# Kernel tuning notes

Measured on AMD Instinct MI355X. Metric: run time of the kernel, lower is better.

## Reference

```python
import jax, jax.numpy as jnp
import numpy as np
from jax import lax

N_PROT = 20000
N_DRUG = 4000
IN_DRUG = 4000
IN_PROT = 64
N_ET = 128
N_BASE = 32
N_EMBED = 48
PD_DIM = 16
H1 = 32
H2 = 16
RGCN_IN = N_EMBED + PD_DIM  # mod='cat'
E_PP = 800000
E_DP = 400000
E_DD = 1000000


def seg_mean(vals, idx, n):
    s = jax.ops.segment_sum(vals, idx, num_segments=n)
    c = jax.ops.segment_sum(jnp.ones(idx.shape, vals.dtype), idx, num_segments=n)
    return s / jnp.maximum(c, 1.0)[:, None]


def gcn(x, W, b, edge_index, n):
    # GCNConv with self-loops and symmetric normalization
    src, dst = edge_index[0], edge_index[1]
    h = x @ W
    deg = jax.ops.segment_sum(jnp.ones(src.shape, h.dtype), dst, num_segments=n) + 1.0
    dis = lax.rsqrt(deg)
    msg = h[src] * (dis[src] * dis[dst])[:, None]
    agg = jax.ops.segment_sum(msg, dst, num_segments=n) + h * (dis * dis)[:, None]
    return agg + b


def rgcn(x, edge_index, etype, att, basis, root, n):
    # message_e = x[src_e] @ (att[etype_e] @ basis) = sum_b att[etype_e, b] * (x[src_e] @ basis[b])
    src, dst = edge_index[0], edge_index[1]
    x_j = x[src]  # [E, in]
    a = att[etype]  # [E, B]
    init = jnp.zeros((src.shape[0], basis.shape[-1]), x.dtype)

    def body(carry, ba):
        basis_b, a_b = ba  # [in,out], [E]
        return carry + a_b[:, None] * (x_j @ basis_b), None

    msgs, _ = lax.scan(body, init, (basis, a.T))
    return seg_mean(msgs, dst, n) + x @ root


def setup_inputs() -> dict:
    key = jax.random.key(0)
    ks = jax.random.split(key, 24)
    x_drug = jax.random.uniform(ks[0], (N_DRUG, IN_DRUG), dtype=jnp.float32)
    d_norm = jax.random.uniform(ks[1], (N_DRUG,), dtype=jnp.float32) + 0.5
    x_prot = jax.random.normal(ks[2], (N_PROT, IN_PROT), dtype=jnp.float32)
    pp_edge_index = jax.random.randint(ks[3], (2, E_PP), 0, N_PROT, dtype=jnp.int32)
    dp_src = jax.random.randint(ks[4], (E_DP,), 0, N_PROT, dtype=jnp.int32)
    dp_dst = N_PROT + jax.random.randint(ks[5], (E_DP,), 0, N_DRUG, dtype=jnp.int32)
    dp_edge_index = jnp.stack([dp_src, dp_dst])
    dp_range_list = jnp.zeros((N_DRUG, 2), dtype=jnp.int32)  # unused in math
    dd_edge_index = jax.random.randint(ks[6], (2, E_DD), 0, N_DRUG, dtype=jnp.int32)
    dd_edge_type = jnp.sort(jax.random.randint(ks[7], (E_DD,), 0, N_ET, dtype=jnp.int32))
    et_np = np.asarray(dd_edge_type)
    starts = np.searchsorted(et_np, np.arange(N_ET), side='left')
    ends = np.searchsorted(et_np, np.arange(N_ET), side='right')
    dd_range_list = jnp.asarray(np.stack([starts, ends], axis=1), dtype=jnp.int32)
    # parameters (init scales per reset_parameters)
    embed = jax.random.normal(ks[8], (IN_DRUG, N_EMBED), dtype=jnp.float32)
    W1 = jax.random.normal(ks[9], (IN_PROT, H1), dtype=jnp.float32) / np.sqrt(IN_PROT)
    b1 = jnp.zeros((H1,), jnp.float32)
    W2 = jax.random.normal(ks[10], (H1, H2), dtype=jnp.float32) / np.sqrt(H1)
    b2 = jnp.zeros((H2,), jnp.float32)
    hg_weight = jax.random.normal(ks[11], (H2, PD_DIM), dtype=jnp.float32) / np.sqrt(H2)
    att1 = jax.random.normal(ks[12], (N_ET, N_BASE), dtype=jnp.float32) / np.sqrt(N_BASE)
    basis1 = jax.random.normal(ks[13], (N_BASE, RGCN_IN, H1), dtype=jnp.float32) / np.sqrt(RGCN_IN)
    root1 = jax.random.normal(ks[14], (RGCN_IN, H1), dtype=jnp.float32) / np.sqrt(RGCN_IN)
    att2 = jax.random.normal(ks[15], (N_ET, N_BASE), dtype=jnp.float32) / np.sqrt(N_BASE)
    basis2 = jax.random.normal(ks[16], (N_BASE, H1, H2), dtype=jnp.float32) * (2.0 / H1)
    root2 = jax.random.normal(ks[17], (H1, H2), dtype=jnp.float32) * (2.0 / H1)
    return {
        'x_drug': x_drug, 'd_norm': d_norm, 'x_prot': x_prot,
        'pp_edge_index': pp_edge_index, 'dp_edge_index': dp_edge_index,
        'dp_range_list': dp_range_list, 'dd_edge_index': dd_edge_index,
        'dd_edge_type': dd_edge_type, 'dd_range_list': dd_range_list,
        'embed': embed, 'W1': W1, 'b1': b1, 'W2': W2, 'b2': b2,
        'hg_weight': hg_weight, 'att1': att1, 'basis1': basis1, 'root1': root1,
        'att2': att2, 'basis2': basis2, 'root2': root2,
    }


def reference(x_drug, d_norm, x_prot, pp_edge_index, dp_edge_index, dp_range_list,
              dd_edge_index, dd_edge_type, dd_range_list, embed, W1, b1, W2, b2,
              hg_weight, att1, basis1, root1, att2, basis2, root2):
    # PPEncoder: two GCN layers
    xp = jax.nn.relu(gcn(x_prot, W1, b1, pp_edge_index, N_PROT))
    xp = gcn(xp, W2, b2, pp_edge_index, N_PROT)  # [N_PROT, H2]
    # MyHierarchyConv: concat zero drug rows, mean-aggregate prot->drug, project
    xcat = jnp.concatenate([xp, jnp.zeros((N_DRUG, H2), xp.dtype)], axis=0)
    agg = seg_mean(xcat[dp_edge_index[0]], dp_edge_index[1], N_PROT + N_DRUG)
    xp_drug = agg[N_PROT:] @ hg_weight  # [N_DRUG, PD_DIM]
    # drug embedding + normalization, concat ('cat' mode)
    xd = (x_drug @ embed) / d_norm[:, None]
    xd = jnp.concatenate([xd, xp_drug], axis=1)  # [N_DRUG, RGCN_IN]
    # two RGCN layers with basis decomposition and mean aggregation
    xd = jax.nn.relu(rgcn(xd, dd_edge_index, dd_edge_type, att1, basis1, root1, N_DRUG))
    xd = rgcn(xd, dd_edge_index, dd_edge_type, att2, basis2, root2, N_DRUG)
    return xd
```

## Files before the change

### kernel.cpp

```cpp
#include <hip/hip_runtime.h>

#define NPROT 20000
#define NDRUG 4000
#define INDRUG 4000
#define NET 128
#define NBASE 32
#define NEMBED 48
#define PDDIM 16
#define H1C 32
#define H2C 16
#define RGCNIN 64
#define EPP 800000
#define EDP 400000
#define EDD 1000000
#define NBLK 256
#define SCANG 8
#define EKCH 160
#define KSPLIT 25
#define PBLKS 4035
#define PEDD (PBLKS*256)

typedef __attribute__((ext_vector_type(8))) __bf16 bf16x8;
typedef __attribute__((ext_vector_type(4))) float f32x4;

__device__ __forceinline__ unsigned int f2bf(float f){
  unsigned int u = __float_as_uint(f);
  u += 0x7fffu + ((u >> 16) & 1u);
  return u >> 16;
}
__device__ __forceinline__ float bf2f(unsigned int s){
  return __uint_as_float(s << 16);
}
__device__ __forceinline__ unsigned long long pack4(const f32x4& c){
  unsigned long long lo = (unsigned long long)(f2bf(c[0]) | (f2bf(c[1]) << 16));
  unsigned long long hi = (unsigned long long)(f2bf(c[2]) | (f2bf(c[3]) << 16));
  return lo | (hi << 32);
}


template<int K, int NC, bool RELU_IN>
__global__ void k_gemm(const float* __restrict__ A, const float* __restrict__ W,
                       float* __restrict__ C, int M){
  __shared__ float Ws[K*NC];
  for(int i = threadIdx.x; i < K*NC; i += 256) Ws[i] = W[i];
  __syncthreads();
  int idx = blockIdx.x*256 + threadIdx.x;
  int row = idx / NC, col = idx % NC;
  if(row >= M) return;
  const float* a = A + row*K;
  float acc = 0.f;
  #pragma unroll
  for(int k = 0; k < K; k++){
    float v = a[k];
    if(RELU_IN) v = fmaxf(v, 0.f);
    acc = fmaf(v, Ws[k*NC + col], acc);
  }
  C[idx] = acc;
}

__global__ void k_gemm_s(const float* __restrict__ A, const float* __restrict__ W,
                         const float* __restrict__ dis, float* __restrict__ C, int M){
  __shared__ float Ws[64*32];
  for(int i = threadIdx.x; i < 64*32; i += 256) Ws[i] = W[i];
  __syncthreads();
  int idx = blockIdx.x*256 + threadIdx.x;
  int row = idx >> 5, col = idx & 31;
  if(row >= M) return;
  const float* a = A + row*64;
  float acc = 0.f;
  #pragma unroll
  for(int k = 0; k < 64; k++)
    acc = fmaf(a[k], Ws[k*32 + col], acc);
  C[idx] = acc * dis[row];
}

__global__ void k_wet(const float* __restrict__ att, const float* __restrict__ basis,
                      float* __restrict__ wet, int inout){
  int gid = blockIdx.x*256 + threadIdx.x;
  if(gid >= NET * inout) return;
  int et = gid / inout, ij = gid % inout;
  float acc = 0.f;
  #pragma unroll
  for(int b = 0; b < NBASE; b++)
    acc = fmaf(att[et*NBASE + b], basis[b*inout + ij], acc);
  wet[gid] = acc;
}

__global__ void k_wetb1(const float* __restrict__ att, const float* __restrict__ basis,
                        unsigned short* __restrict__ wetb){
  int gid = blockIdx.x*256 + threadIdx.x;
  if(gid >= NET*2048) return;
  int et = gid >> 11, r = gid & 2047;
  int f = r >> 9, l = (r >> 3) & 63, j = r & 7;
  int kt = f >> 1, nt = f & 1;
  int k = kt*32 + ((l >> 4) << 3) + j;
  int c = nt*16 + (l & 15);
  float acc = 0.f;
  #pragma unroll
  for(int b = 0; b < NBASE; b++)
    acc = fmaf(att[et*NBASE + b], basis[b*2048 + k*32 + c], acc);
  wetb[gid] = (unsigned short)f2bf(acc);
}

__global__ void k_wetb2(const float* __restrict__ att, const float* __restrict__ basis,
                        unsigned short* __restrict__ wetb){
  int gid = blockIdx.x*256 + threadIdx.x;
  if(gid >= NET*512) return;
  int et = gid >> 9, r = gid & 511;
  int l = r >> 3, j = r & 7;
  int k = ((l >> 4) << 3) + j;
  int c = l & 15;
  float acc = 0.f;
  #pragma unroll
  for(int b = 0; b < NBASE; b++)
    acc = fmaf(att[et*NBASE + b], basis[b*512 + k*16 + c], acc);
  wetb[gid] = (unsigned short)f2bf(acc);
}

__global__ void k_embb(const float* __restrict__ embed, unsigned short* __restrict__ embb){
  int gid = blockIdx.x*256 + threadIdx.x;
  if(gid >= 125*1536) return;
  int kt = gid / 1536, r = gid % 1536;
  int f = r / 512, l = (r >> 3) & 63, j = r & 7;
  int k = kt*32 + ((l >> 4) << 3) + j;
  int c = f*16 + (l & 15);
  embb[gid] = (unsigned short)f2bf(embed[k*48 + c]);
}


__global__ void k_pstart(const int* __restrict__ range, int* __restrict__ pstart,
                         int* __restrict__ pblk){
  __shared__ int ps[NET];
  int t = threadIdx.x;
  int cnt = range[t*2+1] - range[t*2];
  int padc = (cnt + 255) & ~255;
  ps[t] = padc;
  __syncthreads();
  int myoff = 0;
  for(int i = 0; i < t; i++) myoff += ps[i];
  pstart[t] = myoff;
  if(t == NET-1) pstart[NET] = myoff + padc;
  int b0 = myoff >> 8, nb = padc >> 8;
  for(int i = 0; i < nb; i++) pblk[b0 + i] = t;
}

__global__ void k_pmap(const int* __restrict__ et, const int* __restrict__ src,
                       const int* __restrict__ range, const int* __restrict__ pstart,
                       int* __restrict__ psrc, int* __restrict__ pmape){
  int e = blockIdx.x*256 + threadIdx.x;
  if(e >= EDD) return;
  int t = et[e];
  int p = pstart[t] + (e - range[t*2]);
  psrc[p] = src[e];
  pmape[e] = p;
}


template<int PB>
__global__ void k_hist(const int* __restrict__ dst, int ne, int sub, int b0,
                       int* __restrict__ gh, int bins){
  __shared__ int h[PB];
  for(int i = threadIdx.x; i < PB; i += 256) h[i] = 0;
  __syncthreads();
  int chunk = (ne + NBLK - 1) / NBLK;
  int s0 = blockIdx.x*chunk, s1 = min(s0 + chunk, ne);
  for(int i = s0 + threadIdx.x; i < s1; i += 256){
    int b = dst[i] - sub - b0;
    if(b >= 0 && b < PB) atomicAdd(&h[b], 1);
  }
  __syncthreads();
  for(int i = threadIdx.x; i < PB; i += 256) gh[(size_t)blockIdx.x*bins + b0 + i] = h[i];
}

__global__ void k_scan_p1(const int* __restrict__ gh, int* __restrict__ psum, int bins){
  int bin = blockIdx.x*256 + threadIdx.x;
  int g = blockIdx.y;
  if(bin >= bins) return;
  int s = 0;
  #pragma unroll 8
  for(int b = g*32; b < g*32 + 32; b++) s += gh[(size_t)b*bins + bin];
  psum[(size_t)g*bins + bin] = s;
}

__global__ void k_scan_p2(int* __restrict__ gh, const int* __restrict__ psum,
                          int* __restrict__ cnt, int bins){
  int bin = blockIdx.x*256 + threadIdx.x;
  int g = blockIdx.y;
  if(bin >= bins) return;
  int run = 0;
  for(int gg = 0; gg < g; gg++) run += psum[(size_t)gg*bins + bin];
  #pragma unroll 8
  for(int b = g*32; b < g*32 + 32; b++){
    int v = gh[(size_t)b*bins + bin];
    gh[(size_t)b*bins + bin] = run;
    run += v;
  }
  if(g == SCANG-1) cnt[bin] = run;
}

__global__ void k_scan_off(const int* __restrict__ cnt, int* __restrict__ off, int bins){
  __shared__ int ps[1024];
  int t = threadIdx.x;
  int C = (bins + 1023) >> 10;
  int lo = t*C, hi = min(lo + C, bins);
  int s = 0;
  for(int i = lo; i < hi; i++) s += cnt[i];
  ps[t] = s;
  __syncthreads();
  for(int d = 1; d < 1024; d <<= 1){
    int v = (t >= d) ? ps[t-d] : 0;
    __syncthreads();
    ps[t] += v;
    __syncthreads();
  }
  int run = ps[t] - s;
  for(int i = lo; i < hi; i++){ off[i] = run; run += cnt[i]; }
  if(t == 1023) off[bins] = ps[1023];
}

template<int PB, int MODE>
__global__ void k_scatter(const int* __restrict__ dst, const int* __restrict__ src,
                          int ne, int sub, int b0, const int* __restrict__ gh,
                          const int* __restrict__ off, int bins, int* __restrict__ outp){
  __shared__ int h[PB];
  for(int i = threadIdx.x; i < PB; i += 256)
    h[i] = off[b0 + i] + gh[(size_t)blockIdx.x*bins + b0 + i];
  __syncthreads();
  int chunk = (ne + NBLK - 1) / NBLK;
  int s0 = blockIdx.x*chunk, s1 = min(s0 + chunk, ne);
  for(int i = s0 + threadIdx.x; i < s1; i += 256){
    int b = dst[i] - sub - b0;
    if(b >= 0 && b < PB){
      int p = atomicAdd(&h[b], 1);
      outp[p] = src[i];
    }
  }
}

__global__ void k_dis_off(const int* __restrict__ off, float* __restrict__ dis, int n){
  int i = blockIdx.x*256 + threadIdx.x;
  if(i < n) dis[i] = rsqrtf((float)(off[i+1] - off[i]) + 1.0f);
}


__global__ void k_gcn_gather1(const float* __restrict__ hs, const float* __restrict__ dis,
                              const int* __restrict__ off, const int* __restrict__ srcperm,
                              const float* __restrict__ b1, const float* __restrict__ W2,
                              float* __restrict__ h2s){
  __shared__ float red[4][32];
  __shared__ float m[32];
  __shared__ float W2s[512];
  int d = blockIdx.x, tid = threadIdx.x;
  for(int i = tid; i < 512; i += 256) W2s[i] = W2[i];
  int col = tid & 31, g = tid >> 5;
  int o0 = off[d], cnt = off[d+1] - o0;
  float s0 = 0.f, s1 = 0.f, s2 = 0.f, s3 = 0.f;
  int i = g;
  for(; i + 24 < cnt; i += 32){
    int j0 = srcperm[o0 + i],      j1 = srcperm[o0 + i + 8];
    int j2 = srcperm[o0 + i + 16], j3 = srcperm[o0 + i + 24];
    s0 += hs[j0*32 + col]; s1 += hs[j1*32 + col];
    s2 += hs[j2*32 + col]; s3 += hs[j3*32 + col];
  }
  for(; i < cnt; i += 8) s0 += hs[srcperm[o0 + i]*32 + col];
  float s = (s0 + s1) + (s2 + s3);
  s += __shfl_xor(s, 32);
  int wv = tid >> 6, lane = tid & 63;
  if(lane < 32) red[wv][lane] = s;
  __syncthreads();
  float dd = dis[d];
  if(tid < 32){
    float v = (red[0][tid]+red[1][tid]+red[2][tid]+red[3][tid] + hs[d*32 + tid])*dd + b1[tid];
    m[tid] = fmaxf(v, 0.f);
  }
  __syncthreads();
  if(tid < 16){
    float acc = 0.f;
    #pragma unroll
    for(int k = 0; k < 32; k++) acc = fmaf(m[k], W2s[k*16 + tid], acc);
    h2s[d*16 + tid] = acc * dd;
  }
}

__global__ void k_gcn_gather2(const float* __restrict__ hs, const float* __restrict__ dis,
                              const int* __restrict__ off, const int* __restrict__ srcperm,
                              const float* __restrict__ b, float* __restrict__ agg){
  __shared__ float red[4][16];
  int d = blockIdx.x;
  int tid = threadIdx.x;
  int col = tid & 15;
  int g = tid >> 4;
  int o0 = off[d], cnt = off[d+1] - o0;
  float s0 = 0.f, s1 = 0.f;
  int i = g;
  for(; i + 16 < cnt; i += 32){
    int j0 = srcperm[o0 + i], j1 = srcperm[o0 + i + 16];
    s0 += hs[j0*16 + col];
    s1 += hs[j1*16 + col];
  }
  for(; i < cnt; i += 16) s0 += hs[srcperm[o0 + i]*16 + col];
  float s = s0 + s1;
  s += __shfl_xor(s, 32);
  s += __shfl_xor(s, 16);
  int wv = tid >> 6, lane = tid & 63;
  if(lane < 16) red[wv][lane] = s;
  __syncthreads();
  if(tid < 16){
    float tot = red[0][tid] + red[1][tid] + red[2][tid] + red[3][tid];
    float dd = dis[d];
    agg[d*16 + tid] = (tot + hs[d*16 + tid])*dd + b[tid];
  }
}

__global__ void k_dp_gather(const float* __restrict__ xp2, const int* __restrict__ off,
                            const int* __restrict__ srcperm, const float* __restrict__ hg,
                            float* __restrict__ xd, unsigned short* __restrict__ xdb){
  __shared__ float red[4][16];
  __shared__ float m[16];
  int d = blockIdx.x;
  int tid = threadIdx.x;
  int col = tid & 15, g = tid >> 4;
  int o0 = off[d], cnt = off[d+1] - o0;
  float s0 = 0.f, s1 = 0.f, s2 = 0.f, s3 = 0.f;
  int i = g;
  for(; i + 48 < cnt; i += 64){
    int j0 = srcperm[o0 + i],      j1 = srcperm[o0 + i + 16];
    int j2 = srcperm[o0 + i + 32], j3 = srcperm[o0 + i + 48];
    s0 += xp2[j0*16 + col]; s1 += xp2[j1*16 + col];
    s2 += xp2[j2*16 + col]; s3 += xp2[j3*16 + col];
  }
  for(; i < cnt; i += 16) s0 += xp2[srcperm[o0 + i]*16 + col];
  float s = (s0 + s1) + (s2 + s3);
  s += __shfl_xor(s, 32);
  s += __shfl_xor(s, 16);
  int wv = tid >> 6, lane = tid & 63;
  if(lane < 16) red[wv][lane] = s;
  __syncthreads();
  if(tid < 16) m[tid] = (red[0][tid]+red[1][tid]+red[2][tid]+red[3][tid]) / fmaxf((float)cnt, 1.f);
  __syncthreads();
  if(tid < 16){
    float acc = 0.f;
    #pragma unroll
    for(int k = 0; k < 16; k++) acc = fmaf(m[k], hg[k*16 + tid], acc);
    xd[d*64 + 48 + tid] = acc;
    xdb[d*64 + 48 + tid] = (unsigned short)f2bf(acc);
  }
}


__global__ __launch_bounds__(256) void k_embed_m(
    const float* __restrict__ xdrug, const unsigned short* __restrict__ embb,
    float* __restrict__ xdp){
  int tid = threadIdx.x;
  int wv = tid >> 6, l = tid & 63;
  int rt = blockIdx.x*4 + wv;
  int row = rt*16 + (l & 15);
  int kg = (l >> 4) << 3;
  int cb = blockIdx.y * EKCH;
  bool valid = row < NDRUG;
  const float* xr = xdrug + (size_t)row * INDRUG;
  f32x4 z = {0.f,0.f,0.f,0.f};
  f32x4 c0 = z, c1 = z, c2 = z;
  #pragma unroll
  for(int ks = 0; ks < EKCH/32; ks++){
    int k0 = cb + ks*32;
    float4 u = make_float4(0,0,0,0), v = make_float4(0,0,0,0);
    if(valid){
      u = *(const float4*)(xr + k0 + kg);
      v = *(const float4*)(xr + k0 + kg + 4);
    }
    bf16x8 a;
    a[0] = (__bf16)u.x; a[1] = (__bf16)u.y; a[2] = (__bf16)u.z; a[3] = (__bf16)u.w;
    a[4] = (__bf16)v.x; a[5] = (__bf16)v.y; a[6] = (__bf16)v.z; a[7] = (__bf16)v.w;
    const unsigned short* bb = embb + (size_t)(k0 >> 5)*1536 + l*8;
    bf16x8 b0 = *(const bf16x8*)(bb);
    bf16x8 b1 = *(const bf16x8*)(bb + 512);
    bf16x8 b2 = *(const bf16x8*)(bb + 1024);
    c0 = __builtin_amdgcn_mfma_f32_16x16x32_bf16(a, b0, c0, 0,0,0);
    c1 = __builtin_amdgcn_mfma_f32_16x16x32_bf16(a, b1, c1, 0,0,0);
    c2 = __builtin_amdgcn_mfma_f32_16x16x32_bf16(a, b2, c2, 0,0,0);
  }
  int col = l & 15, rb = (l >> 4) << 2;
  float* op = xdp + (size_t)blockIdx.y * NDRUG * 48;
  #pragma unroll
  for(int r = 0; r < 4; r++){
    int ro = rt*16 + rb + r;
    if(ro < NDRUG){
      op[ro*48 + col]       = c0[r];
      op[ro*48 + 16 + col]  = c1[r];
      op[ro*48 + 32 + col]  = c2[r];
    }
  }
}

__global__ void k_embed_fin2(const float* __restrict__ xdp, const float* __restrict__ dnorm,
                             float* __restrict__ xd, unsigned short* __restrict__ xdb){
  int gid = blockIdx.x*256 + threadIdx.x;
  if(gid >= NDRUG*48) return;
  int d = gid / 48, j = gid % 48;
  float s = 0.f;
  for(int y = 0; y < KSPLIT; y++) s += xdp[(size_t)y*NDRUG*48 + gid];
  float v = s / dnorm[d];
  xd[d*64 + j] = v;
  xdb[d*64 + j] = (unsigned short)f2bf(v);
}


__global__ __launch_bounds__(256) void k_rgcn1_msgsM(
    const unsigned short* __restrict__ xdb, const int* __restrict__ psrc,
    const int* __restrict__ pblk, const unsigned short* __restrict__ wetb,
    unsigned short* __restrict__ msgs){
  int tid = threadIdx.x;
  int wv = tid >> 6, l = tid & 63;
  int t0 = pblk[blockIdx.x];
  const unsigned short* wb = wetb + (size_t)t0*2048 + l*8;
  bf16x8 w00 = *(const bf16x8*)(wb);
  bf16x8 w01 = *(const bf16x8*)(wb + 512);
  bf16x8 w10 = *(const bf16x8*)(wb + 1024);
  bf16x8 w11 = *(const bf16x8*)(wb + 1536);
  int eb = blockIdx.x*256 + wv*64;
  int col = l & 15;
  int g4 = (l >> 4) << 3;
  int rb = (l >> 4) << 2;
  int e0 = eb + col, e1 = eb + 16 + col, e2 = eb + 32 + col, e3 = eb + 48 + col;
  int s0 = psrc[e0], s1 = psrc[e1], s2 = psrc[e2], s3 = psrc[e3];
  const unsigned short* x0 = xdb + (size_t)s0*64 + g4;
  const unsigned short* x1 = xdb + (size_t)s1*64 + g4;
  const unsigned short* x2 = xdb + (size_t)s2*64 + g4;
  const unsigned short* x3 = xdb + (size_t)s3*64 + g4;
  bf16x8 a00 = *(const bf16x8*)(x0), a01 = *(const bf16x8*)(x0 + 32);
  bf16x8 a10 = *(const bf16x8*)(x1), a11 = *(const bf16x8*)(x1 + 32);
  bf16x8 a20 = *(const bf16x8*)(x2), a21 = *(const bf16x8*)(x2 + 32);
  bf16x8 a30 = *(const bf16x8*)(x3), a31 = *(const bf16x8*)(x3 + 32);
  f32x4 z = {0.f,0.f,0.f,0.f};
  f32x4 c00=z,c01=z,c10=z,c11=z,c20=z,c21=z,c30=z,c31=z;
  c00 = __builtin_amdgcn_mfma_f32_16x16x32_bf16(w00, a00, c00, 0,0,0);
  c00 = __builtin_amdgcn_mfma_f32_16x16x32_bf16(w10, a01, c00, 0,0,0);
  c01 = __builtin_amdgcn_mfma_f32_16x16x32_bf16(w01, a00, c01, 0,0,0);
  c01 = __builtin_amdgcn_mfma_f32_16x16x32_bf16(w11, a01, c01, 0,0,0);
  c10 = __builtin_amdgcn_mfma_f32_16x16x32_bf16(w00, a10, c10, 0,0,0);
  c10 = __builtin_amdgcn_mfma_f32_16x16x32_bf16(w10, a11, c10, 0,0,0);
  c11 = __builtin_amdgcn_mfma_f32_16x16x32_bf16(w01, a10, c11, 0,0,0);
  c11 = __builtin_amdgcn_mfma_f32_16x16x32_bf16(w11, a11, c11, 0,0,0);
  c20 = __builtin_amdgcn_mfma_f32_16x16x32_bf16(w00, a20, c20, 0,0,0);
  c20 = __builtin_amdgcn_mfma_f32_16x16x32_bf16(w10, a21, c20, 0,0,0);
  c21 = __builtin_amdgcn_mfma_f32_16x16x32_bf16(w01, a20, c21, 0,0,0);
  c21 = __builtin_amdgcn_mfma_f32_16x16x32_bf16(w11, a21, c21, 0,0,0);
  c30 = __builtin_amdgcn_mfma_f32_16x16x32_bf16(w00, a30, c30, 0,0,0);
  c30 = __builtin_amdgcn_mfma_f32_16x16x32_bf16(w10, a31, c30, 0,0,0);
  c31 = __builtin_amdgcn_mfma_f32_16x16x32_bf16(w01, a30, c31, 0,0,0);
  c31 = __builtin_amdgcn_mfma_f32_16x16x32_bf16(w11, a31, c31, 0,0,0);
  *(unsigned long long*)(msgs + (size_t)e0*32 + rb)      = pack4(c00);
  *(unsigned long long*)(msgs + (size_t)e0*32 + 16 + rb) = pack4(c01);
  *(unsigned long long*)(msgs + (size_t)e1*32 + rb)      = pack4(c10);
  *(unsigned long long*)(msgs + (size_t)e1*32 + 16 + rb) = pack4(c11);
  *(unsigned long long*)(msgs + (size_t)e2*32 + rb)      = pack4(c20);
  *(unsigned long long*)(msgs + (size_t)e2*32 + 16 + rb) = pack4(c21);
  *(unsigned long long*)(msgs + (size_t)e3*32 + rb)      = pack4(c30);
  *(unsigned long long*)(msgs + (size_t)e3*32 + 16 + rb) = pack4(c31);
}

__global__ __launch_bounds__(256) void k_rgcn2_msgsM(
    const unsigned short* __restrict__ xd1b, const int* __restrict__ psrc,
    const int* __restrict__ pblk, const unsigned short* __restrict__ wetb,
    unsigned short* __restrict__ msgs){
  int tid = threadIdx.x;
  int wv = tid >> 6, l = tid & 63;
  int t0 = pblk[blockIdx.x];
  bf16x8 w0 = *(const bf16x8*)(wetb + (size_t)t0*512 + l*8);
  int eb = blockIdx.x*256 + wv*64;
  int col = l & 15;
  int g4 = (l >> 4) << 3;
  int rb = (l >> 4) << 2;
  int e0 = eb + col, e1 = eb + 16 + col, e2 = eb + 32 + col, e3 = eb + 48 + col;
  int s0 = psrc[e0], s1 = psrc[e1], s2 = psrc[e2], s3 = psrc[e3];
  bf16x8 a0 = *(const bf16x8*)(xd1b + (size_t)s0*32 + g4);
  bf16x8 a1 = *(const bf16x8*)(xd1b + (size_t)s1*32 + g4);
  bf16x8 a2 = *(const bf16x8*)(xd1b + (size_t)s2*32 + g4);
  bf16x8 a3 = *(const bf16x8*)(xd1b + (size_t)s3*32 + g4);
  f32x4 z = {0.f,0.f,0.f,0.f};
  f32x4 c0=z,c1=z,c2=z,c3=z;
  c0 = __builtin_amdgcn_mfma_f32_16x16x32_bf16(w0, a0, c0, 0,0,0);
  c1 = __builtin_amdgcn_mfma_f32_16x16x32_bf16(w0, a1, c1, 0,0,0);
  c2 = __builtin_amdgcn_mfma_f32_16x16x32_bf16(w0, a2, c2, 0,0,0);
  c3 = __builtin_amdgcn_mfma_f32_16x16x32_bf16(w0, a3, c3, 0,0,0);
  *(unsigned long long*)(msgs + (size_t)e0*16 + rb) = pack4(c0);
  *(unsigned long long*)(msgs + (size_t)e1*16 + rb) = pack4(c1);
  *(unsigned long long*)(msgs + (size_t)e2*16 + rb) = pack4(c2);
  *(unsigned long long*)(msgs + (size_t)e3*16 + rb) = pack4(c3);
}

__global__ void k_rgcn1_reduce(const unsigned short* __restrict__ msgs, const int* __restrict__ off,
                               const int* __restrict__ eperm,
                               const float* __restrict__ xd, const float* __restrict__ root,
                               float* __restrict__ xd1, unsigned short* __restrict__ xd1b){
  __shared__ float red[16][32];
  int d = blockIdx.x;
  int tid = threadIdx.x;
  int cp = tid & 15, r = tid >> 4;
  int o0 = off[d], cnt = off[d+1] - o0;
  float s0 = 0.f, s1 = 0.f;
  int i = r;
  for(; i + 48 < cnt; i += 64){
    int e0 = eperm[o0 + i],      e1 = eperm[o0 + i + 16];
    int e2 = eperm[o0 + i + 32], e3 = eperm[o0 + i + 48];
    unsigned int v0 = *(const unsigned int*)(msgs + (size_t)e0*32 + cp*2);
    unsigned int v1 = *(const unsigned int*)(msgs + (size_t)e1*32 + cp*2);
    unsigned int v2 = *(const unsigned int*)(msgs + (size_t)e2*32 + cp*2);
    unsigned int v3 = *(const unsigned int*)(msgs + (size_t)e3*32 + cp*2);
    s0 += bf2f(v0 & 0xffffu) + bf2f(v1 & 0xffffu) + bf2f(v2 & 0xffffu) + bf2f(v3 & 0xffffu);
    s1 += bf2f(v0 >> 16)     + bf2f(v1 >> 16)     + bf2f(v2 >> 16)     + bf2f(v3 >> 16);
  }
  for(; i < cnt; i += 16){
    int e0 = eperm[o0 + i];
    unsigned int v = *(const unsigned int*)(msgs + (size_t)e0*32 + cp*2);
    s0 += bf2f(v & 0xffffu); s1 += bf2f(v >> 16);
  }
  red[r][cp*2] = s0; red[r][cp*2+1] = s1;
  __syncthreads();
  if(tid < 32){
    float tot = 0.f;
    #pragma unroll
    for(int r2 = 0; r2 < 16; r2++) tot += red[r2][tid];
    float rr = 0.f;
    const float* x = xd + d*64;
    #pragma unroll 8
    for(int i2 = 0; i2 < 64; i2++) rr = fmaf(x[i2], root[i2*32 + tid], rr);
    float v = fmaxf(tot / fmaxf((float)cnt, 1.0f) + rr, 0.f);
    xd1[d*32 + tid] = v;
    xd1b[d*32 + tid] = (unsigned short)f2bf(v);
  }
}

__global__ void k_rgcn2_reduce(const unsigned short* __restrict__ msgs, const int* __restrict__ off,
                               const int* __restrict__ eperm,
                               const float* __restrict__ xd1, const float* __restrict__ root,
                               float* __restrict__ out){
  __shared__ float red[32][16];
  int d = blockIdx.x;
  int tid = threadIdx.x;
  int cp = tid & 7, r = tid >> 3;
  int o0 = off[d], cnt = off[d+1] - o0;
  float s0 = 0.f, s1 = 0.f;
  int i = r;
  for(; i + 96 < cnt; i += 128){
    int e0 = eperm[o0 + i],      e1 = eperm[o0 + i + 32];
    int e2 = eperm[o0 + i + 64], e3 = eperm[o0 + i + 96];
    unsigned int v0 = *(const unsigned int*)(msgs + (size_t)e0*16 + cp*2);
    unsigned int v1 = *(const unsigned int*)(msgs + (size_t)e1*16 + cp*2);
    unsigned int v2 = *(const unsigned int*)(msgs + (size_t)e2*16 + cp*2);
    unsigned int v3 = *(const unsigned int*)(msgs + (size_t)e3*16 + cp*2);
    s0 += bf2f(v0 & 0xffffu) + bf2f(v1 & 0xffffu) + bf2f(v2 & 0xffffu) + bf2f(v3 & 0xffffu);
    s1 += bf2f(v0 >> 16)     + bf2f(v1 >> 16)     + bf2f(v2 >> 16)     + bf2f(v3 >> 16);
  }
  for(; i < cnt; i += 32){
    int e0 = eperm[o0 + i];
    unsigned int v = *(const unsigned int*)(msgs + (size_t)e0*16 + cp*2);
    s0 += bf2f(v & 0xffffu); s1 += bf2f(v >> 16);
  }
  red[r][cp*2] = s0; red[r][cp*2+1] = s1;
  __syncthreads();
  if(tid < 16){
    float tot = 0.f;
    #pragma unroll
    for(int r2 = 0; r2 < 32; r2++) tot += red[r2][tid];
    float rr = 0.f;
    const float* x = xd1 + d*32;
    #pragma unroll 8
    for(int i2 = 0; i2 < 32; i2++) rr = fmaf(x[i2], root[i2*16 + tid], rr);
    out[d*16 + tid] = tot / fmaxf((float)cnt, 1.0f) + rr;
  }
}


#define O_CNTPP   0
#define O_DIS     20000
#define O_H1      40000
#define O_AGG1    680000
#define O_H2      1320000
#define O_AGG2    1640000
#define O_DPSUM   1960000
#define O_DPCNT   2024000
#define O_XD      2028000
#define O_WET1    2284000
#define O_WET2    2546144
#define O_CNTDD   2611680
#define O_RSUM1   2615680
#define O_XD1     2743680
#define O_RSUM2   2871680

__global__ void k_count_int(const int* __restrict__ dst, int ne, int* __restrict__ cnt){
  int i = blockIdx.x*256 + threadIdx.x;
  if(i < ne) atomicAdd(&cnt[dst[i]], 1);
}

__global__ void k_dis(const int* __restrict__ cnt, float* __restrict__ dis, int n){
  int i = blockIdx.x*256 + threadIdx.x;
  if(i < n) dis[i] = rsqrtf((float)cnt[i] + 1.0f);
}

template<int NC>
__global__ void k_gcn_init(const float* __restrict__ h, const float* __restrict__ dis,
                           const float* __restrict__ b, float* __restrict__ agg, int n){
  int i = blockIdx.x*256 + threadIdx.x;
  if(i < n*NC){
    int r = i / NC, c = i % NC;
    float d = dis[r];
    agg[i] = fmaf(h[i], d*d, b[c]);
  }
}

template<int NC>
__global__ void k_gcn_scatter(const float* __restrict__ h, const float* __restrict__ dis,
                              const int* __restrict__ src, const int* __restrict__ dst,
                              int ne, float* __restrict__ agg){
  int gid = blockIdx.x*256 + threadIdx.x;
  int e = gid / NC, j = gid % NC;
  if(e >= ne) return;
  int s = src[e], d = dst[e];
  atomicAdd(&agg[d*NC + j], h[s*NC + j] * dis[s] * dis[d]);
}

__global__ void k_dp_scatter(const float* __restrict__ xp2, const int* __restrict__ src,
                             const int* __restrict__ dst, float* __restrict__ dpsum,
                             int* __restrict__ dpcnt){
  int gid = blockIdx.x*256 + threadIdx.x;
  int e = gid >> 4, j = gid & 15;
  if(e >= EDP) return;
  int s = src[e], d = dst[e] - NPROT;
  atomicAdd(&dpsum[d*16 + j], xp2[s*16 + j]);
  if(j == 0) atomicAdd(&dpcnt[d], 1);
}

__global__ void k_hier(const float* __restrict__ dpsum, const int* __restrict__ dpcnt,
                       const float* __restrict__ hg, float* __restrict__ xd){
  int gid = blockIdx.x*256 + threadIdx.x;
  int d = gid >> 4, j = gid & 15;
  if(d >= NDRUG) return;
  float inv = 1.0f / fmaxf((float)dpcnt[d], 1.0f);
  float acc = 0.f;
  #pragma unroll
  for(int k = 0; k < 16; k++) acc = fmaf(dpsum[d*16 + k] * inv, hg[k*16 + j], acc);
  xd[d*64 + 48 + j] = acc;
}

__global__ void k_embed(const float* __restrict__ xdrug, const float* __restrict__ embed,
                        float* __restrict__ xd){
  __shared__ float xs[64][65];
  __shared__ float es[64][48];
  int tid = threadIdx.x;
  int r = tid & 63;
  int cg = tid >> 6;
  int row0 = blockIdx.x * 64;
  int k0c = blockIdx.y * 512;
  float acc[12];
  #pragma unroll
  for(int j = 0; j < 12; j++) acc[j] = 0.f;
  for(int kt = 0; kt < 512; kt += 64){
    int k0 = k0c + kt;
    if(k0 >= INDRUG) break;
    __syncthreads();
    #pragma unroll
    for(int i = 0; i < 4; i++){
      int lin = tid + i*256;
      int rr = lin >> 4, kc = lin & 15;
      int grow = row0 + rr, gk = k0 + kc*4;
      float4 v = make_float4(0.f,0.f,0.f,0.f);
      if(grow < NDRUG && gk + 3 < INDRUG)
        v = *(const float4*)&xdrug[(size_t)grow * INDRUG + gk];
      xs[rr][kc*4+0]=v.x; xs[rr][kc*4+1]=v.y; xs[rr][kc*4+2]=v.z; xs[rr][kc*4+3]=v.w;
    }
    #pragma unroll
    for(int i = 0; i < 3; i++){
      int lin = tid + i*256;
      int kk = lin / 12, jc = lin % 12;
      float4 v = make_float4(0.f,0.f,0.f,0.f);
      if(k0 + kk < INDRUG)
        v = *(const float4*)&embed[(size_t)(k0 + kk) * NEMBED + jc*4];
      *(float4*)&es[kk][jc*4] = v;
    }
    __syncthreads();
    #pragma unroll 8
    for(int kk = 0; kk < 64; kk++){
      float xv = xs[r][kk];
      const float4* ep = (const float4*)&es[kk][cg*12];
      float4 e0 = ep[0], e1 = ep[1], e2 = ep[2];
      acc[0]=fmaf(xv,e0.x,acc[0]);  acc[1]=fmaf(xv,e0.y,acc[1]);
      acc[2]=fmaf(xv,e0.z,acc[2]);  acc[3]=fmaf(xv,e0.w,acc[3]);
      acc[4]=fmaf(xv,e1.x,acc[4]);  acc[5]=fmaf(xv,e1.y,acc[5]);
      acc[6]=fmaf(xv,e1.z,acc[6]);  acc[7]=fmaf(xv,e1.w,acc[7]);
      acc[8]=fmaf(xv,e2.x,acc[8]);  acc[9]=fmaf(xv,e2.y,acc[9]);
      acc[10]=fmaf(xv,e2.z,acc[10]); acc[11]=fmaf(xv,e2.w,acc[11]);
    }
  }
  int grow = row0 + r;
  if(grow < NDRUG){
    #pragma unroll
    for(int j = 0; j < 12; j++)
      atomicAdd(&xd[grow*64 + cg*12 + j], acc[j]);
  }
}

__global__ void k_embed_fin(float* __restrict__ xd, const float* __restrict__ dnorm){
  int gid = blockIdx.x*256 + threadIdx.x;
  if(gid >= NDRUG*48) return;
  int d = gid / 48, j = gid % 48;
  xd[d*64 + j] = xd[d*64 + j] / dnorm[d];
}

__global__ void k_rgcn1(const float* __restrict__ xd, const int* __restrict__ src,
                        const int* __restrict__ dst, const int* __restrict__ et,
                        const float* __restrict__ wet, float* __restrict__ rsum){
  int tid = threadIdx.x;
  int e = blockIdx.x*64 + (tid >> 2);
  if(e >= EDD) return;
  int jg = tid & 3;
  int s = src[e], d = dst[e], t = et[e];
  const float* x = xd + s*64;
  const float* w = wet + t*2048 + jg*8;
  float acc[8] = {0,0,0,0,0,0,0,0};
  #pragma unroll 8
  for(int i = 0; i < 64; i++){
    float xv = x[i];
    const float4* wp = (const float4*)(w + i*32);
    float4 w0 = wp[0], w1 = wp[1];
    acc[0]=fmaf(xv,w0.x,acc[0]); acc[1]=fmaf(xv,w0.y,acc[1]);
    acc[2]=fmaf(xv,w0.z,acc[2]); acc[3]=fmaf(xv,w0.w,acc[3]);
    acc[4]=fmaf(xv,w1.x,acc[4]); acc[5]=fmaf(xv,w1.y,acc[5]);
    acc[6]=fmaf(xv,w1.z,acc[6]); acc[7]=fmaf(xv,w1.w,acc[7]);
  }
  float* outp = rsum + d*32 + jg*8;
  #pragma unroll
  for(int j = 0; j < 8; j++) atomicAdd(&outp[j], acc[j]);
}

__global__ void k_rgcn2(const float* __restrict__ xd1, const int* __restrict__ src,
                        const int* __restrict__ dst, const int* __restrict__ et,
                        const float* __restrict__ wet, float* __restrict__ rsum){
  int tid = threadIdx.x;
  int e = blockIdx.x*128 + (tid >> 1);
  if(e >= EDD) return;
  int jg = tid & 1;
  int s = src[e], d = dst[e], t = et[e];
  const float* x = xd1 + s*32;
  const float* w = wet + t*512 + jg*8;
  float acc[8] = {0,0,0,0,0,0,0,0};
  #pragma unroll 8
  for(int i = 0; i < 32; i++){
    float xv = x[i];
    const float4* wp = (const float4*)(w + i*16);
    float4 w0 = wp[0], w1 = wp[1];
    acc[0]=fmaf(xv,w0.x,acc[0]); acc[1]=fmaf(xv,w0.y,acc[1]);
    acc[2]=fmaf(xv,w0.z,acc[2]); acc[3]=fmaf(xv,w0.w,acc[3]);
    acc[4]=fmaf(xv,w1.x,acc[4]); acc[5]=fmaf(xv,w1.y,acc[5]);
    acc[6]=fmaf(xv,w1.z,acc[6]); acc[7]=fmaf(xv,w1.w,acc[7]);
  }
  float* outp = rsum + d*16 + jg*8;
  #pragma unroll
  for(int j = 0; j < 8; j++) atomicAdd(&outp[j], acc[j]);
}

__global__ void k_root1(const float* __restrict__ rsum, const int* __restrict__ cnt,
                        const float* __restrict__ xd, const float* __restrict__ root,
                        float* __restrict__ xd1){
  int gid = blockIdx.x*256 + threadIdx.x;
  int d = gid >> 5, j = gid & 31;
  if(d >= NDRUG) return;
  float inv = 1.0f / fmaxf((float)cnt[d], 1.0f);
  float acc = rsum[d*32 + j] * inv;
  #pragma unroll
  for(int i = 0; i < 64; i++) acc = fmaf(xd[d*64 + i], root[i*32 + j], acc);
  xd1[d*32 + j] = fmaxf(acc, 0.f);
}

__global__ void k_root2(const float* __restrict__ rsum, const int* __restrict__ cnt,
                        const float* __restrict__ xd1, const float* __restrict__ root,
                        float* __restrict__ out){
  int gid = blockIdx.x*256 + threadIdx.x;
  int d = gid >> 4, j = gid & 15;
  if(d >= NDRUG) return;
  float inv = 1.0f / fmaxf((float)cnt[d], 1.0f);
  float acc = rsum[d*16 + j] * inv;
  #pragma unroll
  for(int i = 0; i < 32; i++) acc = fmaf(xd1[d*32 + i], root[i*16 + j], acc);
  out[d*16 + j] = acc;
}


extern "C" void kernel_launch(void* const* d_in, const int* in_sizes, int n_in,
                              void* d_out, int out_size, void* d_ws, size_t ws_size,
                              hipStream_t stream){
  const float* x_drug  = (const float*)d_in[0];
  const float* d_norm  = (const float*)d_in[1];
  const float* x_prot  = (const float*)d_in[2];
  const int*   pp_ei   = (const int*)d_in[3];
  const int*   dp_ei   = (const int*)d_in[4];
  const int*   dd_ei   = (const int*)d_in[6];
  const int*   dd_et   = (const int*)d_in[7];
  const int*   dd_rl   = (const int*)d_in[8];
  const float* embed   = (const float*)d_in[9];
  const float* W1      = (const float*)d_in[10];
  const float* b1      = (const float*)d_in[11];
  const float* W2      = (const float*)d_in[12];
  const float* b2      = (const float*)d_in[13];
  const float* hgw     = (const float*)d_in[14];
  const float* att1    = (const float*)d_in[15];
  const float* basis1  = (const float*)d_in[16];
  const float* root1   = (const float*)d_in[17];
  const float* att2    = (const float*)d_in[18];
  const float* basis2  = (const float*)d_in[19];
  const float* root2   = (const float*)d_in[20];
  float* out = (float*)d_out;
  float* ws = (float*)d_ws;

  const int* pp_src = pp_ei;
  const int* pp_dst = pp_ei + EPP;
  const int* dp_src = dp_ei;
  const int* dp_dst = dp_ei + EDP;
  const int* dd_src = dd_ei;
  const int* dd_dst = dd_ei + EDD;

  auto pad = [](size_t n){ return (n + 15) & ~(size_t)15; };
  size_t o = 0;
  size_t oPPOFF = o; o += pad(NPROT + 1);
  size_t oDPOFF = o; o += pad(NDRUG + 1);
  size_t oDDOFF = o; o += pad(NDRUG + 1);
  size_t oDIS   = o; o += pad(NPROT);
  size_t oH1    = o; o += pad((size_t)NPROT*32);
  size_t oH2    = o; o += pad((size_t)NPROT*16);
  size_t oAGG2  = o; o += pad((size_t)NPROT*16);
  size_t oXD    = o; o += pad((size_t)NDRUG*64);
  size_t oXD1   = o; o += pad((size_t)NDRUG*32);
  size_t oXDB   = o; o += pad((size_t)NDRUG*32);
  size_t oXD1B  = o; o += pad((size_t)NDRUG*16);
  size_t oWETB1 = o; o += pad((size_t)NET*1024);
  size_t oWETB2 = o; o += pad((size_t)NET*256);
  size_t oEMBB  = o; o += pad((size_t)125*768);
  size_t oSRCPP = o; o += pad(EPP);
  size_t oSRCDP = o; o += pad(EDP);
  size_t oEPERM = o; o += pad(EDD);
  size_t oPSTART= o; o += pad(NET + 1);
  size_t oPBLK  = o; o += pad(PBLKS);
  size_t oPSRC  = o; o += pad(PEDD);
  size_t oPMAPE = o; o += pad(EDD);
  size_t oCNT   = o; o += pad(NPROT);
  size_t oPSUM  = o; o += pad((size_t)SCANG*NPROT);
  size_t oGH    = o; o += pad((size_t)NBLK*NPROT);
  size_t msgsN  = (size_t)PEDD*16;
  size_t xdpN   = (size_t)KSPLIT*NDRUG*48;
  size_t bigN   = msgsN > xdpN ? msgsN : xdpN;
  size_t oMSGS  = o; o += pad(bigN);
  size_t need_bytes = o * 4;

  if(ws_size >= need_bytes){
    int* ppoff = (int*)(ws + oPPOFF);
    int* dpoff = (int*)(ws + oDPOFF);
    int* ddoff = (int*)(ws + oDDOFF);
    float* dis = ws + oDIS;
    float* h1  = ws + oH1;
    float* h2  = ws + oH2;
    float* agg2= ws + oAGG2;
    float* xd  = ws + oXD;
    float* xd1 = ws + oXD1;
    unsigned short* xdb  = (unsigned short*)(ws + oXDB);
    unsigned short* xd1b = (unsigned short*)(ws + oXD1B);
    unsigned short* wetb1 = (unsigned short*)(ws + oWETB1);
    unsigned short* wetb2 = (unsigned short*)(ws + oWETB2);
    unsigned short* embb  = (unsigned short*)(ws + oEMBB);
    int* srcpp = (int*)(ws + oSRCPP);
    int* srcdp = (int*)(ws + oSRCDP);
    int* eperm = (int*)(ws + oEPERM);
    int* pstart= (int*)(ws + oPSTART);
    int* pblk  = (int*)(ws + oPBLK);
    int* psrc  = (int*)(ws + oPSRC);
    int* pmape = (int*)(ws + oPMAPE);
    int* cnt   = (int*)(ws + oCNT);
    int* psum  = (int*)(ws + oPSUM);
    int* gh    = (int*)(ws + oGH);
    float* xdp = ws + oMSGS;
    unsigned short* msgs = (unsigned short*)(ws + oMSGS);

    hipMemsetAsync(pblk, 0, PBLKS*sizeof(int), stream);
    hipMemsetAsync(psrc, 0, PEDD*sizeof(int), stream);
    k_pstart<<<1,NET,0,stream>>>(dd_rl, pstart, pblk);
    k_pmap<<<(EDD+255)/256,256,0,stream>>>(dd_et, dd_src, dd_rl, pstart, psrc, pmape);

    k_hist<10000><<<NBLK,256,0,stream>>>(pp_dst, EPP, 0, 0,     gh, NPROT);
    k_hist<10000><<<NBLK,256,0,stream>>>(pp_dst, EPP, 0, 10000, gh, NPROT);
    {
      dim3 gs((NPROT+255)/256, SCANG);
      k_scan_p1<<<gs,256,0,stream>>>(gh, psum, NPROT);
      k_scan_p2<<<gs,256,0,stream>>>(gh, psum, cnt, NPROT);
    }
    k_scan_off<<<1,1024,0,stream>>>(cnt, ppoff, NPROT);
    k_scatter<10000,0><<<NBLK,256,0,stream>>>(pp_dst, pp_src, EPP, 0, 0,     gh, ppoff, NPROT, srcpp);
    k_scatter<10000,0><<<NBLK,256,0,stream>>>(pp_dst, pp_src, EPP, 0, 10000, gh, ppoff, NPROT, srcpp);
    k_dis_off<<<(NPROT+255)/256,256,0,stream>>>(ppoff, dis, NPROT);

    k_gemm_s<<<(NPROT*32+255)/256,256,0,stream>>>(x_prot, W1, dis, h1, NPROT);
    k_gcn_gather1<<<NPROT,256,0,stream>>>(h1, dis, ppoff, srcpp, b1, W2, h2);
    k_gcn_gather2<<<NPROT,256,0,stream>>>(h2, dis, ppoff, srcpp, b2, agg2);

    k_hist<4000><<<NBLK,256,0,stream>>>(dp_dst, EDP, NPROT, 0, gh, NDRUG);
    {
      dim3 gs((NDRUG+255)/256, SCANG);
      k_scan_p1<<<gs,256,0,stream>>>(gh, psum, NDRUG);
      k_scan_p2<<<gs,256,0,stream>>>(gh, psum, cnt, NDRUG);
    }
    k_scan_off<<<1,1024,0,stream>>>(cnt, dpoff, NDRUG);
    k_scatter<4000,0><<<NBLK,256,0,stream>>>(dp_dst, dp_src, EDP, NPROT, 0, gh, dpoff, NDRUG, srcdp);
    k_dp_gather<<<NDRUG,256,0,stream>>>(agg2, dpoff, srcdp, hgw, xd, xdb);

    k_embb<<<(125*1536+255)/256,256,0,stream>>>(embed, embb);
    {
      dim3 g(63, KSPLIT);
      k_embed_m<<<g,256,0,stream>>>(x_drug, embb, xdp);
    }
    k_embed_fin2<<<(NDRUG*48+255)/256,256,0,stream>>>(xdp, d_norm, xd, xdb);

    k_wetb1<<<(NET*2048+255)/256,256,0,stream>>>(att1, basis1, wetb1);
    k_wetb2<<<(NET*512+255)/256,256,0,stream>>>(att2, basis2, wetb2);
    k_hist<4000><<<NBLK,256,0,stream>>>(dd_dst, EDD, 0, 0, gh, NDRUG);
    {
      dim3 gs((NDRUG+255)/256, SCANG);
      k_scan_p1<<<gs,256,0,stream>>>(gh, psum, NDRUG);
      k_scan_p2<<<gs,256,0,stream>>>(gh, psum, cnt, NDRUG);
    }
    k_scan_off<<<1,1024,0,stream>>>(cnt, ddoff, NDRUG);
    k_scatter<4000,0><<<NBLK,256,0,stream>>>(dd_dst, pmape, EDD, 0, 0, gh, ddoff, NDRUG, eperm);

    k_rgcn1_msgsM<<<PBLKS,256,0,stream>>>(xdb, psrc, pblk, wetb1, msgs);
    k_rgcn1_reduce<<<NDRUG,256,0,stream>>>(msgs, ddoff, eperm, xd, root1, xd1, xd1b);
    k_rgcn2_msgsM<<<PBLKS,256,0,stream>>>(xd1b, psrc, pblk, wetb2, msgs);
    k_rgcn2_reduce<<<NDRUG,256,0,stream>>>(msgs, ddoff, eperm, xd1, root2, out);
  } else {
    int*   cnt_pp = (int*)(ws + O_CNTPP);
    float* dis    = ws + O_DIS;
    float* h1     = ws + O_H1;
    float* agg1   = ws + O_AGG1;
    float* h2     = ws + O_H2;
    float* agg2   = ws + O_AGG2;
    float* dpsum  = ws + O_DPSUM;
    int*   dpcnt  = (int*)(ws + O_DPCNT);
    float* xd     = ws + O_XD;
    float* wet1   = ws + O_WET1;
    float* wet2   = ws + O_WET2;
    int*   cntdd  = (int*)(ws + O_CNTDD);
    float* rsum1  = ws + O_RSUM1;
    float* xd1    = ws + O_XD1;
    float* rsum2  = ws + O_RSUM2;

    hipMemsetAsync(cnt_pp, 0, NPROT*sizeof(int), stream);
    hipMemsetAsync(dpsum,  0, (64000 + 4000)*sizeof(float), stream);
    hipMemsetAsync(xd,     0, NDRUG*64*sizeof(float), stream);
    hipMemsetAsync(cntdd,  0, NDRUG*sizeof(int), stream);
    hipMemsetAsync(rsum1,  0, NDRUG*32*sizeof(float), stream);
    hipMemsetAsync(rsum2,  0, NDRUG*16*sizeof(float), stream);

    k_count_int<<<(EPP+255)/256,256,0,stream>>>(pp_dst, EPP, cnt_pp);
    k_dis<<<(NPROT+255)/256,256,0,stream>>>(cnt_pp, dis, NPROT);
    k_gemm<64,32,false><<<(NPROT*32+255)/256,256,0,stream>>>(x_prot, W1, h1, NPROT);
    k_gcn_init<32><<<(NPROT*32+255)/256,256,0,stream>>>(h1, dis, b1, agg1, NPROT);
    k_gcn_scatter<32><<<(EPP*32)/256,256,0,stream>>>(h1, dis, pp_src, pp_dst, EPP, agg1);
    k_gemm<32,16,true><<<(NPROT*16+255)/256,256,0,stream>>>(agg1, W2, h2, NPROT);
    k_gcn_init<16><<<(NPROT*16+255)/256,256,0,stream>>>(h2, dis, b2, agg2, NPROT);
    k_gcn_scatter<16><<<(EPP*16)/256,256,0,stream>>>(h2, dis, pp_src, pp_dst, EPP, agg2);
    k_dp_scatter<<<(EDP*16)/256,256,0,stream>>>(agg2, dp_src, dp_dst, dpsum, dpcnt);
    k_hier<<<(NDRUG*16+255)/256,256,0,stream>>>(dpsum, dpcnt, hgw, xd);
    {
      dim3 g((NDRUG+63)/64, 8);
      k_embed<<<g,256,0,stream>>>(x_drug, embed, xd);
    }
    k_embed_fin<<<(NDRUG*48+255)/256,256,0,stream>>>(xd, d_norm);
    k_wet<<<(NET*2048+255)/256,256,0,stream>>>(att1, basis1, wet1, 2048);
    k_wet<<<(NET*512+255)/256,256,0,stream>>>(att2, basis2, wet2, 512);
    k_count_int<<<(EDD+255)/256,256,0,stream>>>(dd_dst, EDD, cntdd);
    k_rgcn1<<<EDD/64,256,0,stream>>>(xd, dd_src, dd_dst, dd_et, wet1, rsum1);
    k_root1<<<(NDRUG*32+255)/256,256,0,stream>>>(rsum1, cntdd, xd, root1, xd1);
    k_rgcn2<<<(EDD+127)/128,256,0,stream>>>(xd1, dd_src, dd_dst, dd_et, wet2, rsum2);
    k_root2<<<(NDRUG*16+255)/256,256,0,stream>>>(rsum2, cntdd, xd1, root2, out);
  }
}
```

Baseline: 353.8 us.

## Scatter RGCN messages directly into destination-sorted order via inverse permutation

The message kernels now write each edge's message to its destination-sorted slot through an inverse permutation built by the scatter kernel, instead of writing in type-sorted order and gathering through eperm. The reduce kernels then read messages contiguously without the indirection load. Padding slots map to a dummy area past EDD via an iota fill. This trades scattered reads in the reduce for scattered 8-byte writes in the message kernels and adds one small init kernel.

New measurement: 342.2 us. -3.3%, faster.

```diff
diff --git a/kernel.cpp b/kernel.cpp
--- a/kernel.cpp
+++ b/kernel.cpp
@@ -155,6 +155,11 @@
   pmape[e] = p;
 }
 
+__global__ void k_iota(int* __restrict__ iperm){
+  int p = blockIdx.x*256 + threadIdx.x;
+  if(p < PEDD) iperm[p] = EDD + (p & 32767);
+}
+
 
 template<int PB>
 __global__ void k_hist(const int* __restrict__ dst, int ne, int sub, int b0,
@@ -232,7 +237,8 @@
     int b = dst[i] - sub - b0;
     if(b >= 0 && b < PB){
       int p = atomicAdd(&h[b], 1);
-      outp[p] = src[i];
+      if(MODE == 0) outp[p] = src[i];
+      else          outp[src[i]] = p;
     }
   }
 }
@@ -409,7 +415,7 @@
 __global__ __launch_bounds__(256) void k_rgcn1_msgsM(
     const unsigned short* __restrict__ xdb, const int* __restrict__ psrc,
     const int* __restrict__ pblk, const unsigned short* __restrict__ wetb,
-    unsigned short* __restrict__ msgs){
+    const int* __restrict__ iperm, unsigned short* __restrict__ msgs){
   int tid = threadIdx.x;
   int wv = tid >> 6, l = tid & 63;
   int t0 = pblk[blockIdx.x];
@@ -424,6 +430,7 @@
   int rb = (l >> 4) << 2;
   int e0 = eb + col, e1 = eb + 16 + col, e2 = eb + 32 + col, e3 = eb + 48 + col;
   int s0 = psrc[e0], s1 = psrc[e1], s2 = psrc[e2], s3 = psrc[e3];
+  int p0 = iperm[e0], p1 = iperm[e1], p2 = iperm[e2], p3 = iperm[e3];
   const unsigned short* x0 = xdb + (size_t)s0*64 + g4;
   const unsigned short* x1 = xdb + (size_t)s1*64 + g4;
   const unsigned short* x2 = xdb + (size_t)s2*64 + g4;
@@ -450,20 +457,20 @@
   c30 = __builtin_amdgcn_mfma_f32_16x16x32_bf16(w10, a31, c30, 0,0,0);
   c31 = __builtin_amdgcn_mfma_f32_16x16x32_bf16(w01, a30, c31, 0,0,0);
   c31 = __builtin_amdgcn_mfma_f32_16x16x32_bf16(w11, a31, c31, 0,0,0);
-  *(unsigned long long*)(msgs + (size_t)e0*32 + rb)      = pack4(c00);
-  *(unsigned long long*)(msgs + (size_t)e0*32 + 16 + rb) = pack4(c01);
-  *(unsigned long long*)(msgs + (size_t)e1*32 + rb)      = pack4(c10);
-  *(unsigned long long*)(msgs + (size_t)e1*32 + 16 + rb) = pack4(c11);
-  *(unsigned long long*)(msgs + (size_t)e2*32 + rb)      = pack4(c20);
-  *(unsigned long long*)(msgs + (size_t)e2*32 + 16 + rb) = pack4(c21);
-  *(unsigned long long*)(msgs + (size_t)e3*32 + rb)      = pack4(c30);
-  *(unsigned long long*)(msgs + (size_t)e3*32 + 16 + rb) = pack4(c31);
+  *(unsigned long long*)(msgs + (size_t)p0*32 + rb)      = pack4(c00);
+  *(unsigned long long*)(msgs + (size_t)p0*32 + 16 + rb) = pack4(c01);
+  *(unsigned long long*)(msgs + (size_t)p1*32 + rb)      = pack4(c10);
+  *(unsigned long long*)(msgs + (size_t)p1*32 + 16 + rb) = pack4(c11);
+  *(unsigned long long*)(msgs + (size_t)p2*32 + rb)      = pack4(c20);
+  *(unsigned long long*)(msgs + (size_t)p2*32 + 16 + rb) = pack4(c21);
+  *(unsigned long long*)(msgs + (size_t)p3*32 + rb)      = pack4(c30);
+  *(unsigned long long*)(msgs + (size_t)p3*32 + 16 + rb) = pack4(c31);
 }
 
 __global__ __launch_bounds__(256) void k_rgcn2_msgsM(
     const unsigned short* __restrict__ xd1b, const int* __restrict__ psrc,
     const int* __restrict__ pblk, const unsigned short* __restrict__ wetb,
-    unsigned short* __restrict__ msgs){
+    const int* __restrict__ iperm, unsigned short* __restrict__ msgs){
   int tid = threadIdx.x;
   int wv = tid >> 6, l = tid & 63;
   int t0 = pblk[blockIdx.x];
@@ -474,6 +481,7 @@
   int rb = (l >> 4) << 2;
   int e0 = eb + col, e1 = eb + 16 + col, e2 = eb + 32 + col, e3 = eb + 48 + col;
   int s0 = psrc[e0], s1 = psrc[e1], s2 = psrc[e2], s3 = psrc[e3];
+  int p0 = iperm[e0], p1 = iperm[e1], p2 = iperm[e2], p3 = iperm[e3];
   bf16x8 a0 = *(const bf16x8*)(xd1b + (size_t)s0*32 + g4);
   bf16x8 a1 = *(const bf16x8*)(xd1b + (size_t)s1*32 + g4);
   bf16x8 a2 = *(const bf16x8*)(xd1b + (size_t)s2*32 + g4);
@@ -484,14 +492,13 @@
   c1 = __builtin_amdgcn_mfma_f32_16x16x32_bf16(w0, a1, c1, 0,0,0);
   c2 = __builtin_amdgcn_mfma_f32_16x16x32_bf16(w0, a2, c2, 0,0,0);
   c3 = __builtin_amdgcn_mfma_f32_16x16x32_bf16(w0, a3, c3, 0,0,0);
-  *(unsigned long long*)(msgs + (size_t)e0*16 + rb) = pack4(c0);
-  *(unsigned long long*)(msgs + (size_t)e1*16 + rb) = pack4(c1);
-  *(unsigned long long*)(msgs + (size_t)e2*16 + rb) = pack4(c2);
-  *(unsigned long long*)(msgs + (size_t)e3*16 + rb) = pack4(c3);
+  *(unsigned long long*)(msgs + (size_t)p0*16 + rb) = pack4(c0);
+  *(unsigned long long*)(msgs + (size_t)p1*16 + rb) = pack4(c1);
+  *(unsigned long long*)(msgs + (size_t)p2*16 + rb) = pack4(c2);
+  *(unsigned long long*)(msgs + (size_t)p3*16 + rb) = pack4(c3);
 }
 
 __global__ void k_rgcn1_reduce(const unsigned short* __restrict__ msgs, const int* __restrict__ off,
-                               const int* __restrict__ eperm,
                                const float* __restrict__ xd, const float* __restrict__ root,
                                float* __restrict__ xd1, unsigned short* __restrict__ xd1b){
   __shared__ float red[16][32];
@@ -502,18 +509,15 @@
   float s0 = 0.f, s1 = 0.f;
   int i = r;
   for(; i + 48 < cnt; i += 64){
-    int e0 = eperm[o0 + i],      e1 = eperm[o0 + i + 16];
-    int e2 = eperm[o0 + i + 32], e3 = eperm[o0 + i + 48];
-    unsigned int v0 = *(const unsigned int*)(msgs + (size_t)e0*32 + cp*2);
-    unsigned int v1 = *(const unsigned int*)(msgs + (size_t)e1*32 + cp*2);
-    unsigned int v2 = *(const unsigned int*)(msgs + (size_t)e2*32 + cp*2);
-    unsigned int v3 = *(const unsigned int*)(msgs + (size_t)e3*32 + cp*2);
+    unsigned int v0 = *(const unsigned int*)(msgs + (size_t)(o0+i)*32 + cp*2);
+    unsigned int v1 = *(const unsigned int*)(msgs + (size_t)(o0+i+16)*32 + cp*2);
+    unsigned int v2 = *(const unsigned int*)(msgs + (size_t)(o0+i+32)*32 + cp*2);
+    unsigned int v3 = *(const unsigned int*)(msgs + (size_t)(o0+i+48)*32 + cp*2);
     s0 += bf2f(v0 & 0xffffu) + bf2f(v1 & 0xffffu) + bf2f(v2 & 0xffffu) + bf2f(v3 & 0xffffu);
     s1 += bf2f(v0 >> 16)     + bf2f(v1 >> 16)     + bf2f(v2 >> 16)     + bf2f(v3 >> 16);
   }
   for(; i < cnt; i += 16){
-    int e0 = eperm[o0 + i];
-    unsigned int v = *(const unsigned int*)(msgs + (size_t)e0*32 + cp*2);
+    unsigned int v = *(const unsigned int*)(msgs + (size_t)(o0+i)*32 + cp*2);
     s0 += bf2f(v & 0xffffu); s1 += bf2f(v >> 16);
   }
   red[r][cp*2] = s0; red[r][cp*2+1] = s1;
@@ -533,7 +537,6 @@
 }
 
 __global__ void k_rgcn2_reduce(const unsigned short* __restrict__ msgs, const int* __restrict__ off,
-                               const int* __restrict__ eperm,
                                const float* __restrict__ xd1, const float* __restrict__ root,
                                float* __restrict__ out){
   __shared__ float red[32][16];
@@ -544,18 +547,15 @@
   float s0 = 0.f, s1 = 0.f;
   int i = r;
   for(; i + 96 < cnt; i += 128){
-    int e0 = eperm[o0 + i],      e1 = eperm[o0 + i + 32];
-    int e2 = eperm[o0 + i + 64], e3 = eperm[o0 + i + 96];
-    unsigned int v0 = *(const unsigned int*)(msgs + (size_t)e0*16 + cp*2);
-    unsigned int v1 = *(const unsigned int*)(msgs + (size_t)e1*16 + cp*2);
-    unsigned int v2 = *(const unsigned int*)(msgs + (size_t)e2*16 + cp*2);
-    unsigned int v3 = *(const unsigned int*)(msgs + (size_t)e3*16 + cp*2);
+    unsigned int v0 = *(const unsigned int*)(msgs + (size_t)(o0+i)*16 + cp*2);
+    unsigned int v1 = *(const unsigned int*)(msgs + (size_t)(o0+i+32)*16 + cp*2);
+    unsigned int v2 = *(const unsigned int*)(msgs + (size_t)(o0+i+64)*16 + cp*2);
+    unsigned int v3 = *(const unsigned int*)(msgs + (size_t)(o0+i+96)*16 + cp*2);
     s0 += bf2f(v0 & 0xffffu) + bf2f(v1 & 0xffffu) + bf2f(v2 & 0xffffu) + bf2f(v3 & 0xffffu);
     s1 += bf2f(v0 >> 16)     + bf2f(v1 >> 16)     + bf2f(v2 >> 16)     + bf2f(v3 >> 16);
   }
   for(; i < cnt; i += 32){
-    int e0 = eperm[o0 + i];
-    unsigned int v = *(const unsigned int*)(msgs + (size_t)e0*16 + cp*2);
+    unsigned int v = *(const unsigned int*)(msgs + (size_t)(o0+i)*16 + cp*2);
     s0 += bf2f(v & 0xffffu); s1 += bf2f(v >> 16);
   }
   red[r][cp*2] = s0; red[r][cp*2+1] = s1;
@@ -838,7 +838,7 @@
   size_t oEMBB  = o; o += pad((size_t)125*768);
   size_t oSRCPP = o; o += pad(EPP);
   size_t oSRCDP = o; o += pad(EDP);
-  size_t oEPERM = o; o += pad(EDD);
+  size_t oIPERM = o; o += pad(PEDD);
   size_t oPSTART= o; o += pad(NET + 1);
   size_t oPBLK  = o; o += pad(PBLKS);
   size_t oPSRC  = o; o += pad(PEDD);
@@ -869,7 +869,7 @@
     unsigned short* embb  = (unsigned short*)(ws + oEMBB);
     int* srcpp = (int*)(ws + oSRCPP);
     int* srcdp = (int*)(ws + oSRCDP);
-    int* eperm = (int*)(ws + oEPERM);
+    int* iperm = (int*)(ws + oIPERM);
     int* pstart= (int*)(ws + oPSTART);
     int* pblk  = (int*)(ws + oPBLK);
     int* psrc  = (int*)(ws + oPSRC);
@@ -884,6 +884,7 @@
     hipMemsetAsync(psrc, 0, PEDD*sizeof(int), stream);
     k_pstart<<<1,NET,0,stream>>>(dd_rl, pstart, pblk);
     k_pmap<<<(EDD+255)/256,256,0,stream>>>(dd_et, dd_src, dd_rl, pstart, psrc, pmape);
+    k_iota<<<(PEDD+255)/256,256,0,stream>>>(iperm);
 
     k_hist<10000><<<NBLK,256,0,stream>>>(pp_dst, EPP, 0, 0,     gh, NPROT);
     k_hist<10000><<<NBLK,256,0,stream>>>(pp_dst, EPP, 0, 10000, gh, NPROT);
@@ -927,12 +928,12 @@
       k_scan_p2<<<gs,256,0,stream>>>(gh, psum, cnt, NDRUG);
     }
     k_scan_off<<<1,1024,0,stream>>>(cnt, ddoff, NDRUG);
-    k_scatter<4000,0><<<NBLK,256,0,stream>>>(dd_dst, pmape, EDD, 0, 0, gh, ddoff, NDRUG, eperm);
-
-    k_rgcn1_msgsM<<<PBLKS,256,0,stream>>>(xdb, psrc, pblk, wetb1, msgs);
-    k_rgcn1_reduce<<<NDRUG,256,0,stream>>>(msgs, ddoff, eperm, xd, root1, xd1, xd1b);
-    k_rgcn2_msgsM<<<PBLKS,256,0,stream>>>(xd1b, psrc, pblk, wetb2, msgs);
-    k_rgcn2_reduce<<<NDRUG,256,0,stream>>>(msgs, ddoff, eperm, xd1, root2, out);
+    k_scatter<4000,1><<<NBLK,256,0,stream>>>(dd_dst, pmape, EDD, 0, 0, gh, ddoff, NDRUG, iperm);
+
+    k_rgcn1_msgsM<<<PBLKS,256,0,stream>>>(xdb, psrc, pblk, wetb1, iperm, msgs);
+    k_rgcn1_reduce<<<NDRUG,256,0,stream>>>(msgs, ddoff, xd, root1, xd1, xd1b);
+    k_rgcn2_msgsM<<<PBLKS,256,0,stream>>>(xd1b, psrc, pblk, wetb2, iperm, msgs);
+    k_rgcn2_reduce<<<NDRUG,256,0,stream>>>(msgs, ddoff, xd1, root2, out);
   } else {
     int*   cnt_pp = (int*)(ws + O_CNTPP);
     float* dis    = ws + O_DIS;
```
